# Performance work log

Hardware: AMD Instinct MI355X
Metric: run time of the kernel (lower is better)

Reference implementation:

```python
import jax, jax.numpy as jnp
import numpy as np

B, T, HID = 2, 512, 1024
H, D, K = 16, 64, 4          # heads, head_dim, short-conv kernel
P = H * D                    # projection_dim
E, TOPK, I, IS = 8, 2, 768, 768  # experts, top_k, expert inter, shared inter
EPS = 1e-5


def setup_inputs() -> dict:
    key = jax.random.key(0)
    ks = jax.random.split(key, 24)
    def r(i, shape, s=0.02):
        return jax.random.normal(ks[i], shape, jnp.float32) * s
    return {
        "x": jax.random.normal(ks[0], (B, T, HID), jnp.float32),
        "norm1_w": jnp.ones((HID,), jnp.float32),
        "wq": r(1, (HID, P)), "wk": r(2, (HID, P)), "wv": r(3, (HID, P)),
        "cq": r(4, (P, K), 0.5), "ck": r(5, (P, K), 0.5), "cv": r(6, (P, K), 0.5),
        "fa": r(7, (HID, D)), "fb": r(8, (D, P)), "bp": r(9, (HID, H)),
        "ga": r(10, (HID, D)), "gb": r(11, (D, P)),
        "A_log": jnp.log(jax.random.uniform(ks[12], (H, 1), jnp.float32, 1.0, 16.0)),
        "dt_bias": r(13, (H, D), 0.1),
        "onorm_w": jnp.ones((D,), jnp.float32),
        "wo": r(14, (P, HID)),
        "norm2_w": jnp.ones((HID,), jnp.float32),
        "gate_w": r(15, (HID, E)), "gate_b": r(16, (E,), 0.1),
        "wg_e": r(17, (E, HID, I)), "wu_e": r(18, (E, HID, I)), "wd_e": r(19, (E, I, HID)),
        "wg_s": r(20, (HID, IS)), "wu_s": r(21, (HID, IS)), "wd_s": r(22, (IS, HID)),
    }


def _rms(x, w, eps=EPS):
    return x * jax.lax.rsqrt(jnp.mean(x * x, axis=-1, keepdims=True) + eps) * w


def _dwconv_silu(x, w):
    # causal depthwise conv, NLC layout: out[b,t,c] = sum_k w[c,k] * x[b, t-(K-1)+k, c]
    xp = jnp.pad(x, ((0, 0), (K - 1, 0), (0, 0)))
    out = sum(w[:, k] * xp[:, k:k + x.shape[1], :] for k in range(K))
    return jax.nn.silu(out)


def _delta_attn(x, wq, wk, wv, cq, ck, cv, fa, fb, bp, ga, gb, A_log, dt_bias, onorm_w, wo):
    q = _dwconv_silu(x @ wq, cq).reshape(B, T, H, D)
    k = _dwconv_silu(x @ wk, ck).reshape(B, T, H, D)
    v = _dwconv_silu(x @ wv, cv).reshape(B, T, H, D)
    # L2-style rms normalization of q/k (no weight, eps=1e-6), then asymmetric scaling
    q = q * jax.lax.rsqrt(jnp.mean(q * q, -1, keepdims=True) + 1e-6)
    k = k * jax.lax.rsqrt(jnp.mean(k * k, -1, keepdims=True) + 1e-6)
    scale = float(D) ** -0.5
    q = (scale ** 2) * q
    k = scale * k
    # fine-grained per-channel gated decay + per-head write strength
    a = ((x @ fa) @ fb).reshape(B, T, H, D)
    g = jnp.exp(-jnp.exp(A_log)[None, None] * jax.nn.softplus(a + dt_bias))  # (B,T,H,D)
    beta = jax.nn.sigmoid(x @ bp)  # (B,T,H)

    def step(S, qkvgb):
        qt, kt, vt, gt, bt = qkvgb            # (B,H,D) each, bt (B,H)
        S = S * gt[..., None]                  # decay over key dim, S: (B,H,Dk,Dv)
        pred = jnp.einsum('bhk,bhkv->bhv', kt, S)
        S = S + jnp.einsum('bhk,bhv->bhkv', kt, (vt - pred) * bt[..., None])
        o = jnp.einsum('bhk,bhkv->bhv', qt, S)
        return S, o

    xs = tuple(jnp.moveaxis(t_, 1, 0) for t_ in (q, k, v, g, beta))
    S0 = jnp.zeros((B, H, D, D), x.dtype)
    _, o = jax.lax.scan(step, S0, xs)
    o = jnp.moveaxis(o, 0, 1)                  # (B,T,H,D)
    gate = ((x @ ga) @ gb).reshape(B, T, H, D)
    o = _rms(o, onorm_w) * jax.nn.sigmoid(gate)
    return o.reshape(B, T, P) @ wo


def _moe(x, gate_w, gate_b, wg_e, wu_e, wd_e, wg_s, wu_s, wd_s):
    n = x.reshape(-1, HID)                     # (N, HID)
    scores = jax.nn.sigmoid(n @ gate_w)        # sigmoid router
    biased = scores + gate_b                   # e_score_correction bias (selection only)
    _, inds = jax.lax.top_k(biased, TOPK)      # n_group==1 -> plain top-k
    w = jnp.take_along_axis(scores, inds, -1)  # gather ORIGINAL scores
    w = w / (w.sum(-1, keepdims=True) + 1e-20) # renormalize; routed_scaling=1.0
    N = n.shape[0]
    comb = jnp.zeros((N, E), n.dtype).at[jnp.arange(N)[:, None], inds].add(w)
    hg = jnp.einsum('nd,edi->eni', n, wg_e)
    hu = jnp.einsum('nd,edi->eni', n, wu_e)
    eo = jnp.einsum('eni,eih->enh', jax.nn.silu(hg) * hu, wd_e)
    routed = jnp.einsum('ne,enh->nh', comb, eo)
    shared = (jax.nn.silu(n @ wg_s) * (n @ wu_s)) @ wd_s
    return (routed + shared).reshape(x.shape)


def _forward(x, norm1_w, wq, wk, wv, cq, ck, cv, fa, fb, bp, ga, gb, A_log, dt_bias,
             onorm_w, wo, norm2_w, gate_w, gate_b, wg_e, wu_e, wd_e, wg_s, wu_s, wd_s):
    h = x + _delta_attn(_rms(x, norm1_w), wq, wk, wv, cq, ck, cv, fa, fb, bp, ga, gb,
                        A_log, dt_bias, onorm_w, wo)
    return h + _moe(_rms(h, norm2_w), gate_w, gate_b, wg_e, wu_e, wd_e, wg_s, wu_s, wd_s)


def reference(x, norm1_w, wq, wk, wv, cq, ck, cv, fa, fb, bp, ga, gb, A_log, dt_bias,
              onorm_w, wo, norm2_w, gate_w, gate_b, wg_e, wu_e, wd_e, wg_s, wu_s, wd_s):
    return _forward(x, norm1_w, wq, wk, wv, cq, ck, cv, fa, fb, bp, ga, gb, A_log,
                    dt_bias, onorm_w, wo, norm2_w, gate_w, gate_b, wg_e, wu_e, wd_e,
                    wg_s, wu_s, wd_s)
```

## Files before the change

### kernel.cpp

```cpp
#include <hip/hip_runtime.h>
#include <hip/hip_bf16.h>
#include <math.h>

#define Bb 2
#define Tt 512
#define HIDD 1024
#define Hh 16
#define Dd 64
#define Pp 1024
#define Kc 4
#define Ee 8
#define Ii 768
#define ISs 768
#define Ntok (Bb*Tt)
#define NASSIGN (2*Ntok)
#define NTOT (NASSIGN + Ntok)
#define SCH 8
#define SNCH (Tt/SCH)

typedef __attribute__((ext_vector_type(8))) short bf16x8;
typedef __attribute__((ext_vector_type(4))) float floatx4;

__device__ __forceinline__ float sigmoidf_(float x){ return 1.f/(1.f+expf(-x)); }
__device__ __forceinline__ float siluf_(float x){ return x/(1.f+expf(-x)); }
__device__ __forceinline__ float bf2f(__hip_bfloat16 b){ return __bfloat162float(b); }

__device__ __forceinline__ void async16(void* lds, const void* g) {
  __builtin_amdgcn_global_load_lds(
      (const __attribute__((address_space(1))) void*)g,
      (__attribute__((address_space(3))) void*)lds, 16, 0, 0);
}

template<int CTRL>
__device__ __forceinline__ float dpp_add(float x){
  int y = __builtin_amdgcn_update_dpp(0, __float_as_int(x), CTRL, 0xF, 0xF, true);
  return x + __int_as_float(y);
}

__device__ __forceinline__ void ds_read128(floatx4& d, const float* p){
  asm volatile("ds_read_b128 %0, %1"
    : "=v"(d)
    : "v"((const __attribute__((address_space(3))) float*)p));
}
__device__ __forceinline__ void ds_read32f(float& d, const float* p){
  asm volatile("ds_read_b32 %0, %1"
    : "=v"(d)
    : "v"((const __attribute__((address_space(3))) float*)p));
}

__global__ void rms_beta_split_kernel(const float* __restrict__ x, const float* __restrict__ w,
                                      const float* __restrict__ bp,
                                      __hip_bfloat16* __restrict__ hi, __hip_bfloat16* __restrict__ lo,
                                      float* __restrict__ betab, float eps) {
  int row = blockIdx.x;
  const float* xr = x + (size_t)row*HIDD;
  float s = 0.f;
  for (int i = threadIdx.x; i < HIDD; i += 256){ float v = xr[i]; s += v*v; }
  #pragma unroll
  for (int off=32; off; off>>=1) s += __shfl_down(s, off, 64);
  __shared__ float red[4];
  if ((threadIdx.x & 63)==0) red[threadIdx.x>>6] = s;
  __syncthreads();
  float tot = red[0]+red[1]+red[2]+red[3];
  float sc = rsqrtf(tot/(float)HIDD + eps);
  float bacc[16] = {};
  for (int i = threadIdx.x; i < HIDD; i += 256) {
    float v = xr[i]*sc*w[i];
    __hip_bfloat16 h = __float2bfloat16(v);
    hi[(size_t)row*HIDD+i] = h;
    lo[(size_t)row*HIDD+i] = __float2bfloat16(v - bf2f(h));
// ... 76 lines not shown

__global__ void trans_inter9_kernel(const float* __restrict__ wg_e, const float* __restrict__ wu_e,
                                    const float* __restrict__ wg_s, const float* __restrict__ wu_s,
                                    __hip_bfloat16* __restrict__ dst) {
  int e = blockIdx.z >> 1, phase = blockIdx.z & 1;
  const float* src = (e < 8) ? ((phase ? wu_e : wg_e) + (size_t)e*HIDD*Ii)
                             : (phase ? wu_s : wg_s);
  dst += (size_t)e*(2*Ii*HIDD);
  __shared__ float tile[32][33];
  int n0 = blockIdx.x*32, k0 = blockIdx.y*32;
  int tx = threadIdx.x & 31, ty0 = threadIdx.x >> 5;
  #pragma unroll
  for (int j=0;j<4;j++){ int ty = ty0 + j*8; tile[ty][tx] = src[(size_t)(k0+ty)*Ii + n0+tx]; }
  __syncthreads();
  #pragma unroll
  for (int j=0;j<4;j++){
    int ty = ty0 + j*8;
    dst[(size_t)(2*(n0+ty)+phase)*HIDD + k0+tx] = __float2bfloat16(tile[tx][ty]);
  }
}

__global__ void trans_down9_kernel(const float* __restrict__ wd_e, const float* __restrict__ wd_s,
                                   __hip_bfloat16* __restrict__ dst) {
  int z = blockIdx.z;
  const float* src = (z < 8) ? wd_e + (size_t)z*Ii*HIDD : wd_s;
  dst += (size_t)z*HIDD*Ii;
  __shared__ float tile[32][33];
  int n0 = blockIdx.x*32, k0 = blockIdx.y*32;
  int tx = threadIdx.x & 31, ty0 = threadIdx.x >> 5;
  #pragma unroll
  for (int j=0;j<4;j++){ int ty = ty0 + j*8; tile[ty][tx] = src[(size_t)(k0+ty)*HIDD + n0+tx]; }
  __syncthreads();
  #pragma unroll
  for (int j=0;j<4;j++){ int ty = ty0 + j*8; dst[(size_t)(n0+ty)*Ii + k0+tx] = __float2bfloat16(tile[tx][ty]); }
}

__device__ __forceinline__ int lds_off(int row, int slot){
  return row*128 + (((slot ^ row)&7)<<4);
}

template<int MODE, int ACC, int BND>
__global__ __launch_bounds__(256)
void gemm_k(const __hip_bfloat16* __restrict__ A, const __hip_bfloat16* __restrict__ BT,
            void* __restrict__ C, int M, int N, int K, int lda, const float* __restrict__ resid,
            const int* __restrict__ counts, const int* __restrict__ prefix,
            const int* __restrict__ ctok, const int* __restrict__ cslot,
            const float* __restrict__ cwt) {
  constexpr int NF = BND/32;
  int Me = M;
  int moff = 0;
  if (MODE == 4 || MODE == 6) {
    int e = blockIdx.z;
    Me = counts[e]; moff = prefix[e];
    A  += (size_t)moff * lda;
    BT += (size_t)e * (size_t)N * K;
  }
  int row0 = blockIdx.y * 64;
  if (row0 >= Me) return;
  int col0 = blockIdx.x * BND;

  __shared__ __attribute__((aligned(16))) short As[64*64];
  __shared__ __attribute__((aligned(16))) short Bs[BND*64];
  const int lane = threadIdx.x & 63;
  const int w    = threadIdx.x >> 6;
  const int wr = w >> 1, wc = w & 1;
  const int srow = lane >> 3;
  const int sch  = (lane & 7) ^ (srow & 7);
  const int q = lane >> 4, r16 = lane & 15;

  const __hip_bfloat16* Ag = A  + (size_t)row0 * lda;
  const __hip_bfloat16* Bg = BT + (size_t)col0 * K;

  floatx4 acc[2][NF] = {};

  for (int k0 = 0; k0 < K; k0 += 64) {
    #pragma unroll
    for (int ii = 0; ii < 2; ++ii) {
      const int inst = w + ii*4;
      const int r = inst*8 + srow;
      async16((char*)As + inst*1024, Ag + (size_t)r*lda + (size_t)(k0 + sch*8));
    }
    #pragma unroll
    for (int ii = 0; ii < BND/32; ++ii) {
      const int inst = w + ii*4;
      const int r = inst*8 + srow;
      async16((char*)Bs + inst*1024, Bg + (size_t)r*K + (size_t)(k0 + sch*8));
    }
    __syncthreads();
    #pragma unroll
    for (int kk = 0; kk < 2; ++kk) {
      int slot = kk*4 + q;
      bf16x8 a0 = *(const bf16x8*)((const char*)As + lds_off(wr*32 +      r16, slot));
      bf16x8 a1 = *(const bf16x8*)((const char*)As + lds_off(wr*32 + 16 + r16, slot));
      bf16x8 b[NF];
      #pragma unroll
      for (int ni=0; ni<NF; ++ni)
        b[ni] = *(const bf16x8*)((const char*)Bs + lds_off(wc*(BND/2) + ni*16 + r16, slot));
      #pragma unroll
      for (int ni=0; ni<NF; ++ni){
        acc[0][ni] = __builtin_amdgcn_mfma_f32_16x16x32_bf16(a0, b[ni], acc[0][ni], 0, 0, 0);
        acc[1][ni] = __builtin_amdgcn_mfma_f32_16x16x32_bf16(a1, b[ni], acc[1][ni], 0, 0, 0);
      }
    }
    __syncthreads();
  }

  #pragma unroll
  for (int mi = 0; mi < 2; ++mi) {
    #pragma unroll
    for (int r = 0; r < 4; ++r) {
      int grow = row0 + wr*32 + mi*16 + q*4 + r;
      if (grow >= Me) continue;
      #pragma unroll
      for (int ni = 0; ni < NF; ++ni) {
        int gcol = col0 + wc*(BND/2) + ni*16 + r16;
        float v = acc[mi][ni][r];
        if (MODE == 1) {
          ((__hip_bfloat16*)C)[(size_t)grow*N + gcol] = __float2bfloat16(v);
        } else if (MODE == 4) {
          int rc = moff + grow;
          int tok = ctok[rc], sl = cslot[rc];
          ((__hip_bfloat16*)C)[((size_t)tok*3 + sl)*N + gcol] = __float2bfloat16(cwt[rc]*v);
        } else if (MODE == 6) {
          float pv = __shfl_xor(v, 1, 64);
          if ((lane & 1) == 0) {
            float rglu = siluf_(v) * pv;
            ((__hip_bfloat16*)C)[(size_t)(moff+grow)*(N/2) + (gcol>>1)] = __float2bfloat16(rglu);
          }
        } else if (MODE == 8) {
          if (gcol < 1024) {
            int hh2 = gcol >> 6, d2 = gcol & 63;
            float t2 = v + cwt[hh2*64 + d2];
            float sp = (t2 > 20.f) ? t2 : log1pf(expf(t2));
            ((float*)C)[(size_t)grow*1024 + gcol] = expf(-expf(resid[hh2]) * sp);
          } else {
            ((float*)(size_t)ctok)[(size_t)grow*1024 + (gcol-1024)] = v;
          }
        }
      }
    }
  }
}

template<int MODE, int BND>
__global__ __launch_bounds__(256)
void gemm3_k(const __hip_bfloat16* __restrict__ Ahi, const __hip_bfloat16* __restrict__ Alo,
             const __hip_bfloat16* __restrict__ Bhi, const __hip_bfloat16* __restrict__ Blo,
             float* __restrict__ C, int M, int N, int K, const float* __restrict__ resid) {
  constexpr int NF = BND/32;
  int row0 = blockIdx.y * 64;
  int col0 = blockIdx.x * BND;

  __shared__ __attribute__((aligned(16))) short As[64*64];
  __shared__ __attribute__((aligned(16))) short Bs[BND*64];
  const int lane = threadIdx.x & 63;
  const int w    = threadIdx.x >> 6;
  const int wr = w >> 1, wc = w & 1;
  const int srow = lane >> 3;
  const int sch  = (lane & 7) ^ (srow & 7);
  const int q = lane >> 4, r16 = lane & 15;

  floatx4 acc[2][NF] = {};

  for (int p = 0; p < 3; ++p) {
    const __hip_bfloat16* Ag = ((p==2)? Alo : Ahi) + (size_t)row0 * K;
    const __hip_bfloat16* Bg = ((p==1)? Blo : Bhi) + (size_t)col0 * K;
    for (int k0 = 0; k0 < K; k0 += 64) {
      #pragma unroll
      for (int ii = 0; ii < 2; ++ii) {
        const int inst = w + ii*4;
        const int r = inst*8 + srow;
        async16((char*)As + inst*1024, Ag + (size_t)r*K + (size_t)(k0 + sch*8));
      }
      #pragma unroll
      for (int ii = 0; ii < BND/32; ++ii) {
        const int inst = w + ii*4;
        const int r = inst*8 + srow;
        async16((char*)Bs + inst*1024, Bg + (size_t)r*K + (size_t)(k0 + sch*8));
      }
      __syncthreads();
      #pragma unroll
      for (int kk = 0; kk < 2; ++kk) {
        int slot = kk*4 + q;
        bf16x8 a0 = *(const bf16x8*)((const char*)As + lds_off(wr*32 +      r16, slot));
        bf16x8 a1 = *(const bf16x8*)((const char*)As + lds_off(wr*32 + 16 + r16, slot));
        bf16x8 b[NF];
        #pragma unroll
        for (int ni=0; ni<NF; ++ni)
          b[ni] = *(const bf16x8*)((const char*)Bs + lds_off(wc*(BND/2) + ni*16 + r16, slot));
        #pragma unroll
        for (int ni=0; ni<NF; ++ni){
          acc[0][ni] = __builtin_amdgcn_mfma_f32_16x16x32_bf16(a0, b[ni], acc[0][ni], 0, 0, 0);
          acc[1][ni] = __builtin_amdgcn_mfma_f32_16x16x32_bf16(a1, b[ni], acc[1][ni], 0, 0, 0);
        }
      }
      __syncthreads();
    }
  }

  #pragma unroll
  for (int mi = 0; mi < 2; ++mi) {
    #pragma unroll
    for (int r = 0; r < 4; ++r) {
      int grow = row0 + wr*32 + mi*16 + q*4 + r;
      #pragma unroll
      for (int ni = 0; ni < NF; ++ni) {
        int gcol = col0 + wc*(BND/2) + ni*16 + r16;
        float v = acc[mi][ni][r];
        if (MODE == 2) v += resid[(size_t)grow*N + gcol];
        C[(size_t)grow*N + gcol] = v;
      }
    }
  }
}

__global__ void conv_norm_kernel(const float* __restrict__ in,
                                 const float* __restrict__ cq, const float* __restrict__ ck,
                                 const float* __restrict__ cv,
                                 float* __restrict__ qc, float* __restrict__ kc,
                                 float* __restrict__ vc) {
  int tok = blockIdx.x;
  int mode = blockIdx.y;
  const float* w = (mode==0) ? cq : (mode==1) ? ck : cv;
  float* outp    = (mode==0) ? qc : (mode==1) ? kc : vc;
  int colOff = mode << 10;
  int t = threadIdx.x;
  int c0 = t*4;
  int tloc = tok & (Tt-1);

  float wv[4][4];
  #pragma unroll
  for (int i=0;i<4;i++){
    float4 w4 = ((const float4*)w)[c0+i];
    wv[i][0]=w4.x; wv[i][1]=w4.y; wv[i][2]=w4.z; wv[i][3]=w4.w;
  }
  float acc[4] = {0.f,0.f,0.f,0.f};
  #pragma unroll
  for (int j=0;j<Kc;j++){
    int tt = tloc - (Kc-1) + j;
    if (tt >= 0){
      float4 xv = *(const float4*)&in[(size_t)(tok-(Kc-1)+j)*3072 + colOff + c0];
      acc[0] += wv[0][j]*xv.x;
      acc[1] += wv[1][j]*xv.y;
      acc[2] += wv[2][j]*xv.z;
      acc[3] += wv[3][j]*xv.w;
    }
  }
  float val[4];
  #pragma unroll
  for (int i=0;i<4;i++) val[i] = siluf_(acc[i]);
  float scale = 1.f;
  if (mode < 2) {
    float ss = val[0]*val[0]+val[1]*val[1]+val[2]*val[2]+val[3]*val[3];
    ss += __shfl_xor(ss, 1, 64);
    ss += __shfl_xor(ss, 2, 64);
    ss += __shfl_xor(ss, 4, 64);
    ss += __shfl_xor(ss, 8, 64);
    scale = rsqrtf(ss/(float)Dd + 1e-6f) * ((mode==0) ? (1.f/64.f) : 0.125f);
  }
  float4 o4 = make_float4(val[0]*scale, val[1]*scale, val[2]*scale, val[3]*scale);
  *(float4*)&outp[(size_t)tok*Pp + c0] = o4;
}

__global__ void moe_rms_scores_kernel(const float* __restrict__ h, const float* __restrict__ w2,
                                      const float* __restrict__ gw,
                                      __hip_bfloat16* __restrict__ hn, float* __restrict__ scores,
                                      int* __restrict__ counts) {
  int row = blockIdx.x;
  if (row == 0 && threadIdx.x < Ee) counts[threadIdx.x] = 0;
  const float* hr = h + (size_t)row*HIDD;
  float s = 0.f;
  for (int i = threadIdx.x; i < HIDD; i += 256){ float v = hr[i]; s += v*v; }
  #pragma unroll
  for (int off=32; off; off>>=1) s += __shfl_down(s, off, 64);
  __shared__ float red[4];
  if ((threadIdx.x & 63)==0) red[threadIdx.x>>6] = s;
  __syncthreads();
  float sc = rsqrtf((red[0]+red[1]+red[2]+red[3])/(float)HIDD + 1e-5f);
  float acc[Ee] = {};
  for (int i = threadIdx.x; i < HIDD; i += 256){
    float xv = hr[i]*sc*w2[i];
    hn[(size_t)row*HIDD + i] = __float2bfloat16(xv);
    #pragma unroll
    for (int e=0;e<Ee;e++) acc[e] += xv*gw[i*Ee+e];
  }
  #pragma unroll
  for (int e=0;e<Ee;e++){
    #pragma unroll
    for (int off=32; off; off>>=1) acc[e] += __shfl_down(acc[e], off, 64);
  }
  __shared__ float red2[4][Ee];
  if ((threadIdx.x & 63)==0){
    #pragma unroll
    for (int e=0;e<Ee;e++) red2[threadIdx.x>>6][e] = acc[e];
  }
  __syncthreads();
  if (threadIdx.x < Ee)
    scores[(size_t)row*Ee + threadIdx.x] =
      red2[0][threadIdx.x]+red2[1][threadIdx.x]+red2[2][threadIdx.x]+red2[3][threadIdx.x];
}

#define REGLOAD(bufi, tbase, K,G,Q,VV,BT) do { \
  const int _b = (bufi); const int _t0 = (tbase); \
  _Pragma("unroll") \
  for (int _i=0;_i<SCH;_i++){ \
    ds_read128(K[_i], &sk[_b][_i][kq*4]); \
    ds_read128(G[_i], &sg[_b][_i][kq*4]); \
    ds_read128(Q[_i], &sq[_b][_i][kq*4]); \
    ds_read32f(VV[_i], &sbv[_t0+_i][vi]); \
    ds_read32f(BT[_i], &sb[_t0+_i]); \
  } \
} while(0)

#define SSTEP(K,G,Q,VV,BT,_i,_t) do { \
  floatx4 k4=K[_i], g4=G[_i], q4=Q[_i]; \
  float vvv=VV[_i], bt=BT[_i]; \
  S0*=g4.x; S1*=g4.y; S2*=g4.z; S3*=g4.w; \
  float pred = S0*k4.x + S1*k4.y + S2*k4.z + S3*k4.w; \
  pred = dpp_add<0xB1>(pred); pred = dpp_add<0x4E>(pred); \
  pred = dpp_add<0x141>(pred); pred = dpp_add<0x140>(pred); \
  float upd = (vvv - pred) * bt; \
  S0 += k4.x*upd; S1 += k4.y*upd; S2 += k4.z*upd; S3 += k4.w*upd; \
  float acc = S0*q4.x + S1*q4.y + S2*q4.z + S3*q4.w; \
  acc = dpp_add<0xB1>(acc); acc = dpp_add<0x4E>(acc); \
  acc = dpp_add<0x141>(acc); acc = dpp_add<0x140>(acc); \
  if (kq == 0) so[_t][vi] = acc; \
} while(0)

#define SITER(c, KC,GC,QC,VC,BC, KN,GN,QN,VN,BN) do { \
  if ((c)+1 < SNCH) { \
    if ((c)+2 < SNCH) asm volatile("s_waitcnt vmcnt(6)" ::: "memory"); \
    else              asm volatile("s_waitcnt vmcnt(0)" ::: "memory"); \
    REGLOAD(((c)+1)%3, ((c)+1)*SCH, KN,GN,QN,VN,BN); \
    if ((c)+3 < SNCH) stage(((c)+3)*SCH, ((c)+3)%3); \
  } \
  _Pragma("unroll") \
  for (int _s=0;_s<SCH;_s++) SSTEP(KC,GC,QC,VC,BC,_s,(c)*SCH+_s); \
  asm volatile("s_waitcnt lgkmcnt(0)" ::: "memory"); \
  __builtin_amdgcn_sched_barrier(0); \
} while(0)

__global__ __launch_bounds__(64)
void scan_kernel(const float* __restrict__ q, const float* __restrict__ k,
                 const float* __restrict__ v, const float* __restrict__ g,
                 const float* __restrict__ beta, float* __restrict__ o) {
  const int vb = blockIdx.x & 15;
  const int hh = (blockIdx.x >> 4) & 15;
  const int b  = blockIdx.x >> 8;
  const int lane = threadIdx.x;
  const int kq = lane & 15;
  const int vi = lane >> 4;
  const int v0 = vb*4;
  const int rb = b*Tt;

  __shared__ __attribute__((aligned(16))) float sq[3][SCH][64];
  __shared__ __attribute__((aligned(16))) float sk[3][SCH][64];
  __shared__ __attribute__((aligned(16))) float sg[3][SCH][64];
  __shared__ __attribute__((aligned(16))) float sbv[Tt][4];
  __shared__ float sb[Tt];
  __shared__ __attribute__((aligned(16))) float so[Tt][4];

  #pragma unroll
  for (int i=0;i<Tt/64;i++)
    sb[i*64+lane] = beta[(size_t)(rb + i*64 + lane)*Hh + hh];
  asm volatile("s_waitcnt vmcnt(0)" ::: "memory");

  #pragma unroll
  for (int i=0;i<Tt/64;i++)
    async16(&sbv[i*64][0], v + (size_t)(rb + i*64 + lane)*Pp + hh*64 + v0);

  auto stage = [&](int t0, int buf) {
    const int srow = lane >> 4, sch4 = (lane & 15)*4;
    #pragma unroll
    for (int ii=0; ii<2; ++ii) {
      size_t gbase = (size_t)(rb + t0 + ii*4 + srow)*Pp + hh*64;
      async16(&sq[buf][ii*4][0], q + gbase + sch4);
      async16(&sk[buf][ii*4][0], k + gbase + sch4);
      async16(&sg[buf][ii*4][0], g + gbase + sch4);
    }
  };

  floatx4 Ka[SCH],Ga[SCH],Qa[SCH], Kb[SCH],Gb[SCH],Qb[SCH];
  float Va[SCH],Bta[SCH], Vb2[SCH],Btb[SCH];
  float S0=0.f,S1=0.f,S2=0.f,S3=0.f;

  stage(0, 0);
  stage(SCH, 1);
  asm volatile("s_waitcnt vmcnt(6)" ::: "memory");
  REGLOAD(0, 0, Ka,Ga,Qa,Va,Bta);
  stage(2*SCH, 2);
  asm volatile("s_waitcnt lgkmcnt(0)" ::: "memory");
  __builtin_amdgcn_sched_barrier(0);

  for (int cp = 0; cp < SNCH; cp += 2) {
    SITER(cp,   Ka,Ga,Qa,Va,Bta, Kb,Gb,Qb,Vb2,Btb);
    SITER(cp+1, Kb,Gb,Qb,Vb2,Btb, Ka,Ga,Qa,Va,Bta);
  }

  #pragma unroll
  for (int i=0;i<Tt/64;i++){
    int t = i*64 + lane;
    *(float4*)&o[(size_t)(rb+t)*Pp + hh*64 + v0] = *(const float4*)&so[t][0];
  }
}

__global__ void onorm_gate_split_kernel(const float* __restrict__ o, const float* __restrict__ w,
                                        const float* __restrict__ gate,
                                        __hip_bfloat16* __restrict__ hi, __hip_bfloat16* __restrict__ lo) {
  int row = blockIdx.x*4 + (threadIdx.x>>6);
  int lane = threadIdx.x & 63;
  size_t idx = (size_t)row*Dd + lane;
  float v = o[idx];
  float s = v*v;
  #pragma unroll
  for (int off=32; off; off>>=1) s += __shfl_xor(s, off, 64);
  float r = v * rsqrtf(s/(float)Dd + 1e-5f) * w[lane] * sigmoidf_(gate[idx]);
  __hip_bfloat16 h = __float2bfloat16(r);
  hi[idx] = h;
  lo[idx] = __float2bfloat16(r - bf2f(h));
}

__global__ void router_kernel(const float* __restrict__ logits, const float* __restrict__ gate_b,
                              int* __restrict__ counts, int* __restrict__ tok_list,
                              int* __restrict__ slot_list, float* __restrict__ wt_list) {
  int n = blockIdx.x*256 + threadIdx.x;
  if (n >= Ntok) return;
  float sc[Ee], bi[Ee];
  #pragma unroll
  for (int e=0;e<Ee;e++){ float s = sigmoidf_(logits[n*Ee+e]); sc[e]=s; bi[e]=s+gate_b[e]; }
  int i0=0;
  #pragma unroll
  for (int e=1;e<Ee;e++) if (bi[e] > bi[i0]) i0=e;
  int i1=-1;
  #pragma unroll
  for (int e=0;e<Ee;e++){ if (e==i0) continue; if (i1<0 || bi[e] > bi[i1]) i1=e; }
  float w0=sc[i0], w1=sc[i1];
  float inv = 1.f/(w0+w1+1e-20f);
  w0*=inv; w1*=inv;
  int p0 = atomicAdd(&counts[i0],1);
  tok_list[i0*Ntok+p0]=n; slot_list[i0*Ntok+p0]=0; wt_list[i0*Ntok+p0]=w0;
  int p1 = atomicAdd(&counts[i1],1);
  tok_list[i1*Ntok+p1]=n; slot_list[i1*Ntok+p1]=1; wt_list[i1*Ntok+p1]=w1;
}

__global__ void compact_kernel(const int* __restrict__ counts, int* __restrict__ prefix,
                               const int* __restrict__ tok_list, const int* __restrict__ slot_list,
                               const float* __restrict__ wt_list,
                               int* __restrict__ ctok, int* __restrict__ cslot, float* __restrict__ cwt,
                               int* __restrict__ counts_mut) {
  int e = blockIdx.x;
  int pe = 0;
  #pragma unroll
  for (int j=0;j<Ee;j++) if (j < e) pe += counts[j];
  if (threadIdx.x == 0) {
    prefix[e] = pe;
    if (e == 0) { prefix[Ee] = NASSIGN; counts_mut[Ee] = Ntok; }
  }
  int c = counts[e];
  for (int i = threadIdx.x; i < c; i += 256) {
    ctok[pe+i]  = tok_list[e*Ntok+i];
    cslot[pe+i] = slot_list[e*Ntok+i];
    cwt[pe+i]   = wt_list[e*Ntok+i];
  }
}

__global__ void gather_kernel(const __hip_bfloat16* __restrict__ hn, int* __restrict__ ctok,
                              int* __restrict__ cslot, float* __restrict__ cwt,
                              __hip_bfloat16* __restrict__ Ae) {
  int r = blockIdx.x;
  int t = threadIdx.x;
  if (r < NASSIGN) {
    ((int4*)(Ae + (size_t)r*HIDD))[t] = ((const int4*)(hn + (size_t)ctok[r]*HIDD))[t];
  } else {
    int tok = r - NASSIGN;
    ((int4*)(Ae + (size_t)r*HIDD))[t] = ((const int4*)(hn + (size_t)tok*HIDD))[t];
    if (t == 0) { ctok[r] = tok; cslot[r] = 2; cwt[r] = 1.f; }
  }
}

__global__ void final_kernel(const float* __restrict__ h, const __hip_bfloat16* __restrict__ routed,
                             float* __restrict__ out) {
  int idx = blockIdx.x*256 + threadIdx.x;
  if (idx >= Ntok*HIDD) return;
  int n = idx >> 10, c = idx & 1023;
  const __hip_bfloat16* rp = routed + (size_t)n*3*HIDD + c;
  out[idx] = h[idx] + bf2f(rp[0]) + bf2f(rp[HIDD]) + bf2f(rp[2*HIDD]);
}

extern "C" void kernel_launch(void* const* d_in, const int* in_sizes, int n_in,
                              void* d_out, int out_size, void* d_ws, size_t ws_size,
                              hipStream_t stream) {
  (void)in_sizes; (void)n_in; (void)out_size; (void)ws_size;
  const float* x        = (const float*)d_in[0];
  const float* norm1_w  = (const float*)d_in[1];
  const float* wq       = (const float*)d_in[2];
  const float* wk       = (const float*)d_in[3];
  const float* wv       = (const float*)d_in[4];
  const float* cq       = (const float*)d_in[5];
  const float* ck       = (const float*)d_in[6];
  const float* cv       = (const float*)d_in[7];
  const float* fa       = (const float*)d_in[8];
  const float* fb       = (const float*)d_in[9];
  const float* bp       = (const float*)d_in[10];
  const float* ga       = (const float*)d_in[11];
  const float* gb       = (const float*)d_in[12];
  const float* A_log    = (const float*)d_in[13];
  const float* dt_bias  = (const float*)d_in[14];
  const float* onorm_w  = (const float*)d_in[15];
  const float* wo       = (const float*)d_in[16];
  const float* norm2_w  = (const float*)d_in[17];
  const float* gate_w   = (const float*)d_in[18];
  const float* gate_b   = (const float*)d_in[19];
  const float* wg_e     = (const float*)d_in[20];
  const float* wu_e     = (const float*)d_in[21];
  const float* wd_e     = (const float*)d_in[22];
  const float* wg_s     = (const float*)d_in[23];
  const float* wu_s     = (const float*)d_in[24];
  const float* wd_s     = (const float*)d_in[25];
  float* out = (float*)d_out;

  char* base = (char*)d_ws;
  size_t off = 0;
  auto alloc = [&](size_t bytes)->char* {
    off = (off + 255) & ~(size_t)255;
    char* p = base + off; off += bytes; return p;
  };
  float* hbuf = (float*)alloc((size_t)Ntok*HIDD*4);
  size_t uStart = (off + 255) & ~(size_t)255;

  off = uStart;
  __hip_bfloat16* xn      = (__hip_bfloat16*)alloc((size_t)Ntok*HIDD*2);
  __hip_bfloat16* xn_lo   = (__hip_bfloat16*)alloc((size_t)Ntok*HIDD*2);
  __hip_bfloat16* wqkv_t  = (__hip_bfloat16*)alloc((size_t)3*Pp*HIDD*2);
  __hip_bfloat16* wqkv_lo = (__hip_bfloat16*)alloc((size_t)3*Pp*HIDD*2);
  float*          qkvlin  = (float*)alloc((size_t)Ntok*3*Pp*4);
  float*          qc      = (float*)alloc((size_t)Ntok*Pp*4);
  float*          kc      = (float*)alloc((size_t)Ntok*Pp*4);
  float*          vc      = (float*)alloc((size_t)Ntok*Pp*4);
  float*          gbuf    = (float*)alloc((size_t)Ntok*Pp*4);
  float*          gatebuf = (float*)alloc((size_t)Ntok*Pp*4);
  float*          obuf    = (float*)alloc((size_t)Ntok*Pp*4);
  __hip_bfloat16* atmp12  = (__hip_bfloat16*)alloc((size_t)Ntok*2*Dd*2);
  float*          betab   = (float*)alloc((size_t)Ntok*Hh*4);
  __hip_bfloat16* obuf_hi = (__hip_bfloat16*)alloc((size_t)Ntok*Pp*2);
  __hip_bfloat16* obuf_lo = (__hip_bfloat16*)alloc((size_t)Ntok*Pp*2);
  __hip_bfloat16* wo_t    = (__hip_bfloat16*)alloc((size_t)HIDD*Pp*2);
  __hip_bfloat16* wo_lo   = (__hip_bfloat16*)alloc((size_t)HIDD*Pp*2);
  __hip_bfloat16* fg_t    = (__hip_bfloat16*)alloc((size_t)2*Dd*HIDD*2);
  __hip_bfloat16* fbgb_t  = (__hip_bfloat16*)alloc((size_t)2048*128*2);

  off = uStart;
  __hip_bfloat16* hn      = (__hip_bfloat16*)alloc((size_t)Ntok*HIDD*2);
  float*          scores  = (float*)alloc((size_t)Ntok*Ee*4);
  int*            counts  = (int*)alloc(64);
  int*            prefix  = (int*)alloc(64);
  int*            tok_list  = (int*)alloc((size_t)Ee*Ntok*4);
  int*            slot_list = (int*)alloc((size_t)Ee*Ntok*4);
  float*          wt_list   = (float*)alloc((size_t)Ee*Ntok*4);
  int*            ctok    = (int*)alloc((size_t)(NTOT+64)*4);
  int*            cslot   = (int*)alloc((size_t)(NTOT+64)*4);
  float*          cwt     = (float*)alloc((size_t)(NTOT+64)*4);
  __hip_bfloat16* egu_t   = (__hip_bfloat16*)alloc((size_t)9*2*Ii*HIDD*2);
  __hip_bfloat16* act     = (__hip_bfloat16*)alloc((size_t)NTOT*Ii*2);
  __hip_bfloat16* routed  = (__hip_bfloat16*)alloc((size_t)Ntok*3*HIDD*2);
  __hip_bfloat16* Ae      = (__hip_bfloat16*)alloc((size_t)NTOT*HIDD*2);
  __hip_bfloat16* ed_t    = (__hip_bfloat16*)alloc((size_t)9*HIDD*Ii*2);

  dim3 blk(256);
  #define NO5 nullptr, nullptr, nullptr, nullptr, nullptr

  rms_beta_split_kernel<<<Ntok, blk, 0, stream>>>(x, norm1_w, bp, xn, xn_lo, betab, 1e-5f);
  trans_split4_kernel<<<dim3(32,32,4), blk, 0, stream>>>(wq, wk, wv, wo,
                                                         wqkv_t, wqkv_lo, wo_t, wo_lo);
  trans_pair_kernel<<<dim3(2,32,2), blk, 0, stream>>>(fa, ga, fg_t, fg_t + (size_t)Dd*HIDD, HIDD, Dd);
  trans_fbgb_kernel<<<dim3(32,2,2), blk, 0, stream>>>(fb, gb, fbgb_t);

  gemm3_k<0,128><<<dim3(24,16,1), blk, 0, stream>>>(xn, xn_lo, wqkv_t, wqkv_lo, qkvlin,
                                                    Ntok, 3*Pp, HIDD, nullptr);
  conv_norm_kernel<<<dim3(Ntok,3,1), blk, 0, stream>>>(qkvlin, cq, ck, cv, qc, kc, vc);
  gemm_k<1,0,64><<<dim3(2,16,1), blk, 0, stream>>>(xn, fg_t, atmp12, Ntok, 2*Dd, HIDD, HIDD, NO5, nullptr);
  gemm_k<8,0,128><<<dim3(16,16,1), blk, 0, stream>>>(atmp12, fbgb_t, gbuf, Ntok, 2048, 128, 2*Dd,
                                                     A_log, nullptr, nullptr,
                                                     (const int*)gatebuf, nullptr, dt_bias);
  scan_kernel<<<Bb*Hh*16, dim3(64), 0, stream>>>(qc, kc, vc, gbuf, betab, obuf);
  onorm_gate_split_kernel<<<(Ntok*Hh)/4, blk, 0, stream>>>(obuf, onorm_w, gatebuf, obuf_hi, obuf_lo);
  gemm3_k<2,64><<<dim3(16,16,1), blk, 0, stream>>>(obuf_hi, obuf_lo, wo_t, wo_lo, hbuf,
                                                   Ntok, HIDD, Pp, x);

  moe_rms_scores_kernel<<<Ntok, blk, 0, stream>>>(hbuf, norm2_w, gate_w, hn, scores, counts);
  router_kernel<<<(Ntok+255)/256, blk, 0, stream>>>(scores, gate_b, counts, tok_list, slot_list, wt_list);
  compact_kernel<<<Ee, blk, 0, stream>>>(counts, prefix, tok_list, slot_list, wt_list,
                                         ctok, cslot, cwt, counts);
  gather_kernel<<<NTOT, dim3(128), 0, stream>>>(hn, ctok, cslot, cwt, Ae);
  trans_inter9_kernel<<<dim3(24,32,18), blk, 0, stream>>>(wg_e, wu_e, wg_s, wu_s, egu_t);
  gemm_k<6,0,128><<<dim3(12,16,9), blk, 0, stream>>>(Ae, egu_t, act, Ntok, 2*Ii, HIDD, HIDD,
                                                     nullptr, counts, prefix, nullptr, nullptr, nullptr);
  trans_down9_kernel<<<dim3(32,24,9), blk, 0, stream>>>(wd_e, wd_s, ed_t);
  gemm_k<4,0,128><<<dim3(8,16,9), blk, 0, stream>>>(act, ed_t, routed, Ntok, HIDD, Ii, Ii,
                                                    nullptr, counts, prefix, ctok, cslot, cwt);

  final_kernel<<<(Ntok*HIDD+255)/256, blk, 0, stream>>>(hbuf, routed, out);
}
```

Baseline: 335.1 us.

## Interleave two heads per scan wavefront to hide serial recurrence latency

The delta-rule scan kernel now handles two heads (h and h+8) per 64-lane block. The two independent recurrences are interleaved step by step, so each head's DPP reduction chain can overlap with the other's. The chunk size is halved (SCH 8→4) so the staging still issues six async loads per stage and the vmcnt waits stay valid. The grid shrinks from 512 to 256 blocks, and LDS and register use per block roughly double, which may reduce occupancy and parallelism.

After: 374.4 us. 11.7% more time.

```diff
diff --git a/kernel.cpp b/kernel.cpp
--- a/kernel.cpp
+++ b/kernel.cpp
@@ -15,7 +15,7 @@
 #define Ntok (Bb*Tt)
 #define NASSIGN (2*Ntok)
 #define NTOT (NASSIGN + Ntok)
-#define SCH 8
+#define SCH 4
 #define SNCH (Tt/SCH)
 
 typedef __attribute__((ext_vector_type(8))) short bf16x8;
@@ -446,42 +446,55 @@
       red2[0][threadIdx.x]+red2[1][threadIdx.x]+red2[2][threadIdx.x]+red2[3][threadIdx.x];
 }
 
-#define REGLOAD(bufi, tbase, K,G,Q,VV,BT) do { \
+#define REGLOAD2(bufi, tbase, K,G,Q,VV,BT) do { \
   const int _b = (bufi); const int _t0 = (tbase); \
   _Pragma("unroll") \
-  for (int _i=0;_i<SCH;_i++){ \
-    ds_read128(K[_i], &sk[_b][_i][kq*4]); \
-    ds_read128(G[_i], &sg[_b][_i][kq*4]); \
-    ds_read128(Q[_i], &sq[_b][_i][kq*4]); \
-    ds_read32f(VV[_i], &sbv[_t0+_i][vi]); \
-    ds_read32f(BT[_i], &sb[_t0+_i]); \
+  for (int _h=0;_h<2;_h++){ \
+    _Pragma("unroll") \
+    for (int _i=0;_i<SCH;_i++){ \
+      ds_read128(K[_h][_i], &sk[_h][_b][_i][kq*4]); \
+      ds_read128(G[_h][_i], &sg[_h][_b][_i][kq*4]); \
+      ds_read128(Q[_h][_i], &sq[_h][_b][_i][kq*4]); \
+      ds_read32f(VV[_h][_i], &sbv[_h][_t0+_i][vi]); \
+      ds_read32f(BT[_h][_i], &sb[_h][_t0+_i]); \
+    } \
   } \
 } while(0)
 
-#define SSTEP(K,G,Q,VV,BT,_i,_t) do { \
-  floatx4 k4=K[_i], g4=G[_i], q4=Q[_i]; \
-  float vvv=VV[_i], bt=BT[_i]; \
-  S0*=g4.x; S1*=g4.y; S2*=g4.z; S3*=g4.w; \
-  float pred = S0*k4.x + S1*k4.y + S2*k4.z + S3*k4.w; \
-  pred = dpp_add<0xB1>(pred); pred = dpp_add<0x4E>(pred); \
-  pred = dpp_add<0x141>(pred); pred = dpp_add<0x140>(pred); \
-  float upd = (vvv - pred) * bt; \
-  S0 += k4.x*upd; S1 += k4.y*upd; S2 += k4.z*upd; S3 += k4.w*upd; \
-  float acc = S0*q4.x + S1*q4.y + S2*q4.z + S3*q4.w; \
-  acc = dpp_add<0xB1>(acc); acc = dpp_add<0x4E>(acc); \
-  acc = dpp_add<0x141>(acc); acc = dpp_add<0x140>(acc); \
-  if (kq == 0) so[_t][vi] = acc; \
+#define SSTEP2(K,G,Q,VV,BT,_i,_t) do { \
+  floatx4 k40=K[0][_i], g40=G[0][_i], q40=Q[0][_i]; \
+  floatx4 k41=K[1][_i], g41=G[1][_i], q41=Q[1][_i]; \
+  float vv0=VV[0][_i], bt0=BT[0][_i], vv1=VV[1][_i], bt1=BT[1][_i]; \
+  S0*=g40.x; T0*=g41.x; S1*=g40.y; T1*=g41.y; \
+  S2*=g40.z; T2*=g41.z; S3*=g40.w; T3*=g41.w; \
+  float p0 = S0*k40.x + S1*k40.y + S2*k40.z + S3*k40.w; \
+  float p1 = T0*k41.x + T1*k41.y + T2*k41.z + T3*k41.w; \
+  p0 = dpp_add<0xB1>(p0);  p1 = dpp_add<0xB1>(p1); \
+  p0 = dpp_add<0x4E>(p0);  p1 = dpp_add<0x4E>(p1); \
+  p0 = dpp_add<0x141>(p0); p1 = dpp_add<0x141>(p1); \
+  p0 = dpp_add<0x140>(p0); p1 = dpp_add<0x140>(p1); \
+  float u0 = (vv0 - p0) * bt0; \
+  float u1 = (vv1 - p1) * bt1; \
+  S0 += k40.x*u0; T0 += k41.x*u1; S1 += k40.y*u0; T1 += k41.y*u1; \
+  S2 += k40.z*u0; T2 += k41.z*u1; S3 += k40.w*u0; T3 += k41.w*u1; \
+  float a0 = S0*q40.x + S1*q40.y + S2*q40.z + S3*q40.w; \
+  float a1 = T0*q41.x + T1*q41.y + T2*q41.z + T3*q41.w; \
+  a0 = dpp_add<0xB1>(a0);  a1 = dpp_add<0xB1>(a1); \
+  a0 = dpp_add<0x4E>(a0);  a1 = dpp_add<0x4E>(a1); \
+  a0 = dpp_add<0x141>(a0); a1 = dpp_add<0x141>(a1); \
+  a0 = dpp_add<0x140>(a0); a1 = dpp_add<0x140>(a1); \
+  if (kq == 0) { so[0][_t][vi] = a0; so[1][_t][vi] = a1; } \
 } while(0)
 
-#define SITER(c, KC,GC,QC,VC,BC, KN,GN,QN,VN,BN) do { \
+#define SITER2(c, KC,GC,QC,VC,BC, KN,GN,QN,VN,BN) do { \
   if ((c)+1 < SNCH) { \
     if ((c)+2 < SNCH) asm volatile("s_waitcnt vmcnt(6)" ::: "memory"); \
     else              asm volatile("s_waitcnt vmcnt(0)" ::: "memory"); \
-    REGLOAD(((c)+1)%3, ((c)+1)*SCH, KN,GN,QN,VN,BN); \
+    REGLOAD2(((c)+1)%3, ((c)+1)*SCH, KN,GN,QN,VN,BN); \
     if ((c)+3 < SNCH) stage(((c)+3)*SCH, ((c)+3)%3); \
   } \
   _Pragma("unroll") \
-  for (int _s=0;_s<SCH;_s++) SSTEP(KC,GC,QC,VC,BC,_s,(c)*SCH+_s); \
+  for (int _s=0;_s<SCH;_s++) SSTEP2(KC,GC,QC,VC,BC,_s,(c)*SCH+_s); \
   asm volatile("s_waitcnt lgkmcnt(0)" ::: "memory"); \
   __builtin_amdgcn_sched_barrier(0); \
 } while(0)
@@ -491,62 +504,70 @@
                  const float* __restrict__ v, const float* __restrict__ g,
                  const float* __restrict__ beta, float* __restrict__ o) {
   const int vb = blockIdx.x & 15;
-  const int hh = (blockIdx.x >> 4) & 15;
-  const int b  = blockIdx.x >> 8;
+  const int hh = (blockIdx.x >> 4) & 7;
+  const int b  = blockIdx.x >> 7;
   const int lane = threadIdx.x;
   const int kq = lane & 15;
   const int vi = lane >> 4;
   const int v0 = vb*4;
   const int rb = b*Tt;
-
-  __shared__ __attribute__((aligned(16))) float sq[3][SCH][64];
-  __shared__ __attribute__((aligned(16))) float sk[3][SCH][64];
-  __shared__ __attribute__((aligned(16))) float sg[3][SCH][64];
-  __shared__ __attribute__((aligned(16))) float sbv[Tt][4];
-  __shared__ float sb[Tt];
-  __shared__ __attribute__((aligned(16))) float so[Tt][4];
-
-  #pragma unroll
-  for (int i=0;i<Tt/64;i++)
-    sb[i*64+lane] = beta[(size_t)(rb + i*64 + lane)*Hh + hh];
+  const int h0 = hh, h1 = hh + 8;
+
+  __shared__ __attribute__((aligned(16))) float sq[2][3][SCH][64];
+  __shared__ __attribute__((aligned(16))) float sk[2][3][SCH][64];
+  __shared__ __attribute__((aligned(16))) float sg[2][3][SCH][64];
+  __shared__ __attribute__((aligned(16))) float sbv[2][Tt][4];
+  __shared__ float sb[2][Tt];
+  __shared__ __attribute__((aligned(16))) float so[2][Tt][4];
+
+  #pragma unroll
+  for (int i=0;i<Tt/64;i++){
+    sb[0][i*64+lane] = beta[(size_t)(rb + i*64 + lane)*Hh + h0];
+    sb[1][i*64+lane] = beta[(size_t)(rb + i*64 + lane)*Hh + h1];
+  }
   asm volatile("s_waitcnt vmcnt(0)" ::: "memory");
 
   #pragma unroll
-  for (int i=0;i<Tt/64;i++)
-    async16(&sbv[i*64][0], v + (size_t)(rb + i*64 + lane)*Pp + hh*64 + v0);
+  for (int i=0;i<Tt/64;i++){
+    async16(&sbv[0][i*64][0], v + (size_t)(rb + i*64 + lane)*Pp + h0*64 + v0);
+    async16(&sbv[1][i*64][0], v + (size_t)(rb + i*64 + lane)*Pp + h1*64 + v0);
+  }
 
   auto stage = [&](int t0, int buf) {
     const int srow = lane >> 4, sch4 = (lane & 15)*4;
-    #pragma unroll
-    for (int ii=0; ii<2; ++ii) {
-      size_t gbase = (size_t)(rb + t0 + ii*4 + srow)*Pp + hh*64;
-      async16(&sq[buf][ii*4][0], q + gbase + sch4);
-      async16(&sk[buf][ii*4][0], k + gbase + sch4);
-      async16(&sg[buf][ii*4][0], g + gbase + sch4);
-    }
+    size_t gbase0 = (size_t)(rb + t0 + srow)*Pp + h0*64 + sch4;
+    size_t gbase1 = (size_t)(rb + t0 + srow)*Pp + h1*64 + sch4;
+    async16(&sq[0][buf][0][0], q + gbase0);
+    async16(&sq[1][buf][0][0], q + gbase1);
+    async16(&sk[0][buf][0][0], k + gbase0);
+    async16(&sk[1][buf][0][0], k + gbase1);
+    async16(&sg[0][buf][0][0], g + gbase0);
+    async16(&sg[1][buf][0][0], g + gbase1);
   };
 
-  floatx4 Ka[SCH],Ga[SCH],Qa[SCH], Kb[SCH],Gb[SCH],Qb[SCH];
-  float Va[SCH],Bta[SCH], Vb2[SCH],Btb[SCH];
+  floatx4 Ka[2][SCH],Ga[2][SCH],Qa[2][SCH], Kb[2][SCH],Gb[2][SCH],Qb[2][SCH];
+  float Va[2][SCH],Bta[2][SCH], Vb2[2][SCH],Btb[2][SCH];
   float S0=0.f,S1=0.f,S2=0.f,S3=0.f;
+  float T0=0.f,T1=0.f,T2=0.f,T3=0.f;
 
   stage(0, 0);
   stage(SCH, 1);
   asm volatile("s_waitcnt vmcnt(6)" ::: "memory");
-  REGLOAD(0, 0, Ka,Ga,Qa,Va,Bta);
+  REGLOAD2(0, 0, Ka,Ga,Qa,Va,Bta);
   stage(2*SCH, 2);
   asm volatile("s_waitcnt lgkmcnt(0)" ::: "memory");
   __builtin_amdgcn_sched_barrier(0);
 
   for (int cp = 0; cp < SNCH; cp += 2) {
-    SITER(cp,   Ka,Ga,Qa,Va,Bta, Kb,Gb,Qb,Vb2,Btb);
-    SITER(cp+1, Kb,Gb,Qb,Vb2,Btb, Ka,Ga,Qa,Va,Bta);
+    SITER2(cp,   Ka,Ga,Qa,Va,Bta, Kb,Gb,Qb,Vb2,Btb);
+    SITER2(cp+1, Kb,Gb,Qb,Vb2,Btb, Ka,Ga,Qa,Va,Bta);
   }
 
   #pragma unroll
   for (int i=0;i<Tt/64;i++){
     int t = i*64 + lane;
-    *(float4*)&o[(size_t)(rb+t)*Pp + hh*64 + v0] = *(const float4*)&so[t][0];
+    *(float4*)&o[(size_t)(rb+t)*Pp + h0*64 + v0] = *(const float4*)&so[0][t][0];
+    *(float4*)&o[(size_t)(rb+t)*Pp + h1*64 + v0] = *(const float4*)&so[1][t][0];
   }
 }
 
@@ -728,7 +749,7 @@
   gemm_k<8,0,128><<<dim3(16,16,1), blk, 0, stream>>>(atmp12, fbgb_t, gbuf, Ntok, 2048, 128, 2*Dd,
                                                      A_log, nullptr, nullptr,
                                                      (const int*)gatebuf, nullptr, dt_bias);
-  scan_kernel<<<Bb*Hh*16, dim3(64), 0, stream>>>(qc, kc, vc, gbuf, betab, obuf);
+  scan_kernel<<<Bb*8*16, dim3(64), 0, stream>>>(qc, kc, vc, gbuf, betab, obuf);
   onorm_gate_split_kernel<<<(Ntok*Hh)/4, blk, 0, stream>>>(obuf, onorm_w, gatebuf, obuf_hi, obuf_lo);
   gemm3_k<2,64><<<dim3(16,16,1), blk, 0, stream>>>(obuf_hi, obuf_lo, wo_t, wo_lo, hbuf,
                                                    Ntok, HIDD, Pp, x);
```

## Fuse MoE routing into one kernel, gather rows inside GEMM, merge split-precision passes

Applied to the files above, without the earlier changes.

Router, compaction and gather kernels are replaced by a single 1024-thread block that computes the top-2 assignments, prefix offsets and the compacted token lists using shared-memory atomics. The expert gate/up GEMM then loads A rows indirectly through a token index table in LDS, so the materialized gathered activation buffer is no longer needed. The three-pass hi/lo split GEMM is restructured so the Ahi tile is loaded once and multiplied against both Bhi and Blo, which cuts A-tile reloads at the cost of extra LDS. Risks include a serial single-block router, and the gathered loads being less coalesced and depending on the index reads.

Result: faster. 311.5 us (-7.1%).

```diff
diff --git a/kernel.cpp b/kernel.cpp
--- a/kernel.cpp
+++ b/kernel.cpp
@@ -198,7 +198,7 @@
   if (MODE == 4 || MODE == 6) {
     int e = blockIdx.z;
     Me = counts[e]; moff = prefix[e];
-    A  += (size_t)moff * lda;
+    if (MODE == 4) A += (size_t)moff * lda;
     BT += (size_t)e * (size_t)N * K;
   }
   int row0 = blockIdx.y * 64;
@@ -207,6 +207,7 @@
 
   __shared__ __attribute__((aligned(16))) short As[64*64];
   __shared__ __attribute__((aligned(16))) short Bs[BND*64];
+  __shared__ int sidx[64];
   const int lane = threadIdx.x & 63;
   const int w    = threadIdx.x >> 6;
   const int wr = w >> 1, wc = w & 1;
@@ -214,6 +215,14 @@
   const int sch  = (lane & 7) ^ (srow & 7);
   const int q = lane >> 4, r16 = lane & 15;
 
+  if (MODE == 6) {
+    if (threadIdx.x < 64) {
+      int rr = row0 + threadIdx.x;
+      sidx[threadIdx.x] = (rr < Me) ? ctok[moff + rr] : 0;
+    }
+    __syncthreads();
+  }
+
   const __hip_bfloat16* Ag = A  + (size_t)row0 * lda;
   const __hip_bfloat16* Bg = BT + (size_t)col0 * K;
 
@@ -224,7 +233,10 @@
     for (int ii = 0; ii < 2; ++ii) {
       const int inst = w + ii*4;
       const int r = inst*8 + srow;
-      async16((char*)As + inst*1024, Ag + (size_t)r*lda + (size_t)(k0 + sch*8));
+      if (MODE == 6)
+        async16((char*)As + inst*1024, A + (size_t)sidx[r]*lda + (size_t)(k0 + sch*8));
+      else
+        async16((char*)As + inst*1024, Ag + (size_t)r*lda + (size_t)(k0 + sch*8));
     }
     #pragma unroll
     for (int ii = 0; ii < BND/32; ++ii) {
@@ -298,7 +310,7 @@
   int col0 = blockIdx.x * BND;
 
   __shared__ __attribute__((aligned(16))) short As[64*64];
-  __shared__ __attribute__((aligned(16))) short Bs[BND*64];
+  __shared__ __attribute__((aligned(16))) short Bs[2][BND*64];
   const int lane = threadIdx.x & 63;
   const int w    = threadIdx.x >> 6;
   const int wr = w >> 1, wc = w & 1;
@@ -306,42 +318,78 @@
   const int sch  = (lane & 7) ^ (srow & 7);
   const int q = lane >> 4, r16 = lane & 15;
 
+  const __hip_bfloat16* Ag0 = Ahi + (size_t)row0 * K;
+  const __hip_bfloat16* Ag1 = Alo + (size_t)row0 * K;
+  const __hip_bfloat16* Bg0 = Bhi + (size_t)col0 * K;
+  const __hip_bfloat16* Bg1 = Blo + (size_t)col0 * K;
+
   floatx4 acc[2][NF] = {};
 
-  for (int p = 0; p < 3; ++p) {
-    const __hip_bfloat16* Ag = ((p==2)? Alo : Ahi) + (size_t)row0 * K;
-    const __hip_bfloat16* Bg = ((p==1)? Blo : Bhi) + (size_t)col0 * K;
-    for (int k0 = 0; k0 < K; k0 += 64) {
+  for (int k0 = 0; k0 < K; k0 += 64) {
+    #pragma unroll
+    for (int ii = 0; ii < 2; ++ii) {
+      const int inst = w + ii*4;
+      const int r = inst*8 + srow;
+      async16((char*)As + inst*1024, Ag0 + (size_t)r*K + (size_t)(k0 + sch*8));
+    }
+    #pragma unroll
+    for (int ii = 0; ii < BND/32; ++ii) {
+      const int inst = w + ii*4;
+      const int r = inst*8 + srow;
+      async16((char*)Bs[0] + inst*1024, Bg0 + (size_t)r*K + (size_t)(k0 + sch*8));
+      async16((char*)Bs[1] + inst*1024, Bg1 + (size_t)r*K + (size_t)(k0 + sch*8));
+    }
+    __syncthreads();
+    #pragma unroll
+    for (int kk = 0; kk < 2; ++kk) {
+      int slot = kk*4 + q;
+      bf16x8 a0 = *(const bf16x8*)((const char*)As + lds_off(wr*32 +      r16, slot));
+      bf16x8 a1 = *(const bf16x8*)((const char*)As + lds_off(wr*32 + 16 + r16, slot));
       #pragma unroll
-      for (int ii = 0; ii < 2; ++ii) {
-        const int inst = w + ii*4;
-        const int r = inst*8 + srow;
-        async16((char*)As + inst*1024, Ag + (size_t)r*K + (size_t)(k0 + sch*8));
-      }
-      #pragma unroll
-      for (int ii = 0; ii < BND/32; ++ii) {
-        const int inst = w + ii*4;
-        const int r = inst*8 + srow;
-        async16((char*)Bs + inst*1024, Bg + (size_t)r*K + (size_t)(k0 + sch*8));
-      }
-      __syncthreads();
-      #pragma unroll
-      for (int kk = 0; kk < 2; ++kk) {
-        int slot = kk*4 + q;
-        bf16x8 a0 = *(const bf16x8*)((const char*)As + lds_off(wr*32 +      r16, slot));
-        bf16x8 a1 = *(const bf16x8*)((const char*)As + lds_off(wr*32 + 16 + r16, slot));
+      for (int pb = 0; pb < 2; ++pb) {
         bf16x8 b[NF];
         #pragma unroll
         for (int ni=0; ni<NF; ++ni)
-          b[ni] = *(const bf16x8*)((const char*)Bs + lds_off(wc*(BND/2) + ni*16 + r16, slot));
+          b[ni] = *(const bf16x8*)((const char*)Bs[pb] + lds_off(wc*(BND/2) + ni*16 + r16, slot));
         #pragma unroll
         for (int ni=0; ni<NF; ++ni){
           acc[0][ni] = __builtin_amdgcn_mfma_f32_16x16x32_bf16(a0, b[ni], acc[0][ni], 0, 0, 0);
           acc[1][ni] = __builtin_amdgcn_mfma_f32_16x16x32_bf16(a1, b[ni], acc[1][ni], 0, 0, 0);
         }
       }
-      __syncthreads();
-    }
+    }
+    __syncthreads();
+  }
+  for (int k0 = 0; k0 < K; k0 += 64) {
+    #pragma unroll
+    for (int ii = 0; ii < 2; ++ii) {
+      const int inst = w + ii*4;
+      const int r = inst*8 + srow;
+      async16((char*)As + inst*1024, Ag1 + (size_t)r*K + (size_t)(k0 + sch*8));
+    }
+    #pragma unroll
+    for (int ii = 0; ii < BND/32; ++ii) {
+      const int inst = w + ii*4;
+      const int r = inst*8 + srow;
+      async16((char*)Bs[0] + inst*1024, Bg0 + (size_t)r*K + (size_t)(k0 + sch*8));
+    }
+    __syncthreads();
+    #pragma unroll
+    for (int kk = 0; kk < 2; ++kk) {
+      int slot = kk*4 + q;
+      bf16x8 a0 = *(const bf16x8*)((const char*)As + lds_off(wr*32 +      r16, slot));
+      bf16x8 a1 = *(const bf16x8*)((const char*)As + lds_off(wr*32 + 16 + r16, slot));
+      bf16x8 b[NF];
+      #pragma unroll
+      for (int ni=0; ni<NF; ++ni)
+        b[ni] = *(const bf16x8*)((const char*)Bs[0] + lds_off(wc*(BND/2) + ni*16 + r16, slot));
+      #pragma unroll
+      for (int ni=0; ni<NF; ++ni){
+        acc[0][ni] = __builtin_amdgcn_mfma_f32_16x16x32_bf16(a0, b[ni], acc[0][ni], 0, 0, 0);
+        acc[1][ni] = __builtin_amdgcn_mfma_f32_16x16x32_bf16(a1, b[ni], acc[1][ni], 0, 0, 0);
+      }
+    }
+    __syncthreads();
   }
 
   #pragma unroll
@@ -410,10 +458,8 @@
 
 __global__ void moe_rms_scores_kernel(const float* __restrict__ h, const float* __restrict__ w2,
                                       const float* __restrict__ gw,
-                                      __hip_bfloat16* __restrict__ hn, float* __restrict__ scores,
-                                      int* __restrict__ counts) {
+                                      __hip_bfloat16* __restrict__ hn, float* __restrict__ scores) {
   int row = blockIdx.x;
-  if (row == 0 && threadIdx.x < Ee) counts[threadIdx.x] = 0;
   const float* hr = h + (size_t)row*HIDD;
   float s = 0.f;
   for (int i = threadIdx.x; i < HIDD; i += 256){ float v = hr[i]; s += v*v; }
@@ -566,11 +612,16 @@
   lo[idx] = __float2bfloat16(r - bf2f(h));
 }
 
-__global__ void router_kernel(const float* __restrict__ logits, const float* __restrict__ gate_b,
-                              int* __restrict__ counts, int* __restrict__ tok_list,
-                              int* __restrict__ slot_list, float* __restrict__ wt_list) {
-  int n = blockIdx.x*256 + threadIdx.x;
-  if (n >= Ntok) return;
+__global__ void router_compact_kernel(const float* __restrict__ logits, const float* __restrict__ gate_b,
+                                      int* __restrict__ counts, int* __restrict__ prefix,
+                                      int* __restrict__ ctok, int* __restrict__ cslot,
+                                      float* __restrict__ cwt) {
+  int n = threadIdx.x;
+  __shared__ int scnt[Ee];
+  __shared__ int spre[Ee];
+  __shared__ int soff[Ee];
+  if (n < Ee) { scnt[n] = 0; soff[n] = 0; }
+  __syncthreads();
   float sc[Ee], bi[Ee];
   #pragma unroll
   for (int e=0;e<Ee;e++){ float s = sigmoidf_(logits[n*Ee+e]); sc[e]=s; bi[e]=s+gate_b[e]; }
@@ -583,45 +634,18 @@
   float w0=sc[i0], w1=sc[i1];
   float inv = 1.f/(w0+w1+1e-20f);
   w0*=inv; w1*=inv;
-  int p0 = atomicAdd(&counts[i0],1);
-  tok_list[i0*Ntok+p0]=n; slot_list[i0*Ntok+p0]=0; wt_list[i0*Ntok+p0]=w0;
-  int p1 = atomicAdd(&counts[i1],1);
-  tok_list[i1*Ntok+p1]=n; slot_list[i1*Ntok+p1]=1; wt_list[i1*Ntok+p1]=w1;
-}
-
-__global__ void compact_kernel(const int* __restrict__ counts, int* __restrict__ prefix,
-                               const int* __restrict__ tok_list, const int* __restrict__ slot_list,
-                               const float* __restrict__ wt_list,
-                               int* __restrict__ ctok, int* __restrict__ cslot, float* __restrict__ cwt,
-                               int* __restrict__ counts_mut) {
-  int e = blockIdx.x;
-  int pe = 0;
-  #pragma unroll
-  for (int j=0;j<Ee;j++) if (j < e) pe += counts[j];
-  if (threadIdx.x == 0) {
-    prefix[e] = pe;
-    if (e == 0) { prefix[Ee] = NASSIGN; counts_mut[Ee] = Ntok; }
-  }
-  int c = counts[e];
-  for (int i = threadIdx.x; i < c; i += 256) {
-    ctok[pe+i]  = tok_list[e*Ntok+i];
-    cslot[pe+i] = slot_list[e*Ntok+i];
-    cwt[pe+i]   = wt_list[e*Ntok+i];
-  }
-}
-
-__global__ void gather_kernel(const __hip_bfloat16* __restrict__ hn, int* __restrict__ ctok,
-                              int* __restrict__ cslot, float* __restrict__ cwt,
-                              __hip_bfloat16* __restrict__ Ae) {
-  int r = blockIdx.x;
-  int t = threadIdx.x;
-  if (r < NASSIGN) {
-    ((int4*)(Ae + (size_t)r*HIDD))[t] = ((const int4*)(hn + (size_t)ctok[r]*HIDD))[t];
-  } else {
-    int tok = r - NASSIGN;
-    ((int4*)(Ae + (size_t)r*HIDD))[t] = ((const int4*)(hn + (size_t)tok*HIDD))[t];
-    if (t == 0) { ctok[r] = tok; cslot[r] = 2; cwt[r] = 1.f; }
-  }
+  atomicAdd(&scnt[i0],1);
+  atomicAdd(&scnt[i1],1);
+  __syncthreads();
+  if (n == 0){ int s=0; for (int e=0;e<Ee;e++){ spre[e]=s; s+=scnt[e]; } }
+  __syncthreads();
+  int p0 = spre[i0] + atomicAdd(&soff[i0],1);
+  ctok[p0]=n; cslot[p0]=0; cwt[p0]=w0;
+  int p1 = spre[i1] + atomicAdd(&soff[i1],1);
+  ctok[p1]=n; cslot[p1]=1; cwt[p1]=w1;
+  ctok[NASSIGN+n]=n; cslot[NASSIGN+n]=2; cwt[NASSIGN+n]=1.f;
+  if (n < Ee){ counts[n]=scnt[n]; prefix[n]=spre[n]; }
+  if (n == 0){ counts[Ee]=Ntok; prefix[Ee]=NASSIGN; }
 }
 
 __global__ void final_kernel(const float* __restrict__ h, const __hip_bfloat16* __restrict__ routed,
@@ -700,16 +724,12 @@
   float*          scores  = (float*)alloc((size_t)Ntok*Ee*4);
   int*            counts  = (int*)alloc(64);
   int*            prefix  = (int*)alloc(64);
-  int*            tok_list  = (int*)alloc((size_t)Ee*Ntok*4);
-  int*            slot_list = (int*)alloc((size_t)Ee*Ntok*4);
-  float*          wt_list   = (float*)alloc((size_t)Ee*Ntok*4);
   int*            ctok    = (int*)alloc((size_t)(NTOT+64)*4);
   int*            cslot   = (int*)alloc((size_t)(NTOT+64)*4);
   float*          cwt     = (float*)alloc((size_t)(NTOT+64)*4);
   __hip_bfloat16* egu_t   = (__hip_bfloat16*)alloc((size_t)9*2*Ii*HIDD*2);
   __hip_bfloat16* act     = (__hip_bfloat16*)alloc((size_t)NTOT*Ii*2);
   __hip_bfloat16* routed  = (__hip_bfloat16*)alloc((size_t)Ntok*3*HIDD*2);
-  __hip_bfloat16* Ae      = (__hip_bfloat16*)alloc((size_t)NTOT*HIDD*2);
   __hip_bfloat16* ed_t    = (__hip_bfloat16*)alloc((size_t)9*HIDD*Ii*2);
 
   dim3 blk(256);
@@ -733,14 +753,12 @@
   gemm3_k<2,64><<<dim3(16,16,1), blk, 0, stream>>>(obuf_hi, obuf_lo, wo_t, wo_lo, hbuf,
                                                    Ntok, HIDD, Pp, x);
 
-  moe_rms_scores_kernel<<<Ntok, blk, 0, stream>>>(hbuf, norm2_w, gate_w, hn, scores, counts);
-  router_kernel<<<(Ntok+255)/256, blk, 0, stream>>>(scores, gate_b, counts, tok_list, slot_list, wt_list);
-  compact_kernel<<<Ee, blk, 0, stream>>>(counts, prefix, tok_list, slot_list, wt_list,
-                                         ctok, cslot, cwt, counts);
-  gather_kernel<<<NTOT, dim3(128), 0, stream>>>(hn, ctok, cslot, cwt, Ae);
+  moe_rms_scores_kernel<<<Ntok, blk, 0, stream>>>(hbuf, norm2_w, gate_w, hn, scores);
+  router_compact_kernel<<<1, dim3(1024), 0, stream>>>(scores, gate_b, counts, prefix,
+                                                      ctok, cslot, cwt);
   trans_inter9_kernel<<<dim3(24,32,18), blk, 0, stream>>>(wg_e, wu_e, wg_s, wu_s, egu_t);
-  gemm_k<6,0,128><<<dim3(12,16,9), blk, 0, stream>>>(Ae, egu_t, act, Ntok, 2*Ii, HIDD, HIDD,
-                                                     nullptr, counts, prefix, nullptr, nullptr, nullptr);
+  gemm_k<6,0,128><<<dim3(12,16,9), blk, 0, stream>>>(hn, egu_t, act, Ntok, 2*Ii, HIDD, HIDD,
+                                                     nullptr, counts, prefix, ctok, nullptr, nullptr);
   trans_down9_kernel<<<dim3(32,24,9), blk, 0, stream>>>(wd_e, wd_s, ed_t);
   gemm_k<4,0,128><<<dim3(8,16,9), blk, 0, stream>>>(act, ed_t, routed, Ntok, HIDD, Ii, Ii,
                                                     nullptr, counts, prefix, ctok, cslot, cwt);
```
